# Optimization experiments

Hardware: AMD Instinct MI355X
Metric: run time of the kernel (lower is better)

Reference implementation:

```python
import jax, jax.numpy as jnp
import numpy as np

B, S, DIM, H, D = 2, 2048, 1024, 16, 64
WINDOW = 512
MAX_MEM_SEGMENTS = 1
ROPE_THETA = 10000.0


def _rope(t, pos):
    # lucidrains rotary-embedding-torch default: interleaved pairs
    d = t.shape[-1]
    inv_freq = 1.0 / (ROPE_THETA ** (jnp.arange(0, d, 2, dtype=jnp.float32) / d))
    freqs = pos[:, None].astype(jnp.float32) * inv_freq[None, :]        # [S, d/2]
    freqs = jnp.repeat(freqs, 2, axis=-1)                               # [S, d]
    cos, sin = jnp.cos(freqs), jnp.sin(freqs)
    t1, t2 = t[..., 0::2], t[..., 1::2]
    rot = jnp.stack((-t2, t1), axis=-1).reshape(t.shape)                # rotate_half
    return t * cos + rot * sin


def setup_inputs() -> dict:
    key = jax.random.key(0)
    ks = jax.random.split(key, 8)
    tokens = jax.random.normal(ks[0], (B, S, DIM), dtype=jnp.float32)
    value_residual = jax.random.normal(ks[1], (B, H, S, D), dtype=jnp.float32)
    episode_ids = jnp.sort(jax.random.randint(ks[2], (B, S), 0, 4), axis=-1)
    w = 0.02
    Wq = jax.random.normal(ks[3], (DIM, H * D), dtype=jnp.float32) * w
    Wkv = jax.random.normal(ks[4], (DIM, 2 * H * D), dtype=jnp.float32) * w
    Wo = jax.random.normal(ks[5], (H * D, DIM), dtype=jnp.float32) * w
    Wg = jax.random.normal(ks[6], (DIM, H), dtype=jnp.float32) * w
    Wmix = jax.random.normal(ks[7], (DIM, H), dtype=jnp.float32) * w
    return {"tokens": tokens, "value_residual": value_residual, "episode_ids": episode_ids,
            "Wq": Wq, "Wkv": Wkv, "Wo": Wo, "Wg": Wg, "Wmix": Wmix}


def reference(tokens, value_residual, episode_ids, Wq, Wkv, Wo, Wg, Wmix):
    b, s, _ = tokens.shape
    scale = D ** -0.5

    def split_heads(x):  # [b, n, h*d] -> [b, h, n, d]
        return x.reshape(b, s, H, D).transpose(0, 2, 1, 3)

    q = split_heads(tokens @ Wq)
    kv = tokens @ Wkv
    k, v = split_heads(kv[..., :H * D]), split_heads(kv[..., H * D:])

    q = q * scale

    # value-residual lerp: v.lerp(value_residual, mix)
    mix = jax.nn.sigmoid(jnp.einsum('bnd,dh->bhn', tokens, Wmix))[..., None]  # [b,h,n,1]
    v = v + mix * (value_residual - v)

    pos = jnp.arange(s)
    q = _rope(q, pos)
    k = _rope(k, pos)

    sim = jnp.einsum('bhid,bhjd->bhij', q, k)

    # fixed-window causal mask: masked where dist < 0 or dist > max_mem_segments*window
    dist = pos[:, None] - pos[None, :]
    win_mask = (dist < 0) | (dist > MAX_MEM_SEGMENTS * WINDOW)            # [s, s]
    ep_mask = episode_ids[:, :, None] != episode_ids[:, None, :]          # [b, s, s]
    mask = win_mask[None, None, :, :] | ep_mask[:, None, :, :]

    sim = jnp.where(mask, -jnp.finfo(sim.dtype).max, sim)
    attn = jax.nn.softmax(sim, axis=-1)
    out = jnp.einsum('bhij,bhjd->bhid', attn, v)

    # sigmoid value gating
    gate = jax.nn.sigmoid(jnp.einsum('bnd,dh->bhn', tokens, Wg))[..., None]
    out = out * gate

    out = out.transpose(0, 2, 1, 3).reshape(b, s, H * D)
    return out @ Wo
```

## Files before the change

### kernel.cpp

```cpp
#include <hip/hip_runtime.h>
#include <math.h>

#define BB 2
#define SS 2048
#define DIMM 1024
#define HH 16
#define DD 64
#define WINDOW 512

typedef __bf16 bf16x8 __attribute__((ext_vector_type(8)));
typedef float f32x4 __attribute__((ext_vector_type(4)));

__device__ __forceinline__ unsigned short f2bf(float f) {
    unsigned int u = __float_as_uint(f);
    u = (u + 0x7FFFu + ((u >> 16) & 1u)) >> 16;
    return (unsigned short)u;
}
__device__ __forceinline__ float bf2f(unsigned short u) {
    return __uint_as_float((unsigned int)u << 16);
}

__device__ __forceinline__ void async_cp16(unsigned short* lds_dst, const unsigned short* g_src) {
    __builtin_amdgcn_global_load_lds(
        (const __attribute__((address_space(1))) unsigned int*)g_src,
        (__attribute__((address_space(3))) unsigned int*)lds_dst, 16, 0, 0);
}

__global__ __launch_bounds__(256) void cvt_bf16_kernel(
    const float* __restrict__ src, unsigned short* __restrict__ dst, int n4)
{
    for (int i = blockIdx.x * 256 + threadIdx.x; i < n4; i += gridDim.x * 256) {
        float4 v = ((const float4*)src)[i];
        ushort4 o;
        o.x = f2bf(v.x); o.y = f2bf(v.y); o.z = f2bf(v.z); o.w = f2bf(v.w);
        ((ushort4*)dst)[i] = o;
    }
}

__global__ __launch_bounds__(256) void transpose_cvt3_kernel(
    const float* __restrict__ Wq, const float* __restrict__ Wkv,
    const float* __restrict__ Wo, unsigned short* __restrict__ BtW,
    unsigned short* __restrict__ WotW)
{
    int z = blockIdx.z;
    const float* src = (z == 0) ? Wq : (z == 1) ? Wkv : Wo;
    unsigned short* dst = (z == 0) ? BtW : (z == 1) ? (BtW + 1024 * 1024) : WotW;
    int C = (z == 1) ? 2048 : 1024;
    if (blockIdx.x * 32 >= C) return;
    const int R = 1024;

    __shared__ float t[32][33];
    int c0 = blockIdx.x * 32, r0 = blockIdx.y * 32;
    int tx = threadIdx.x & 31, ty = threadIdx.x >> 5;
    #pragma unroll
    for (int u = 0; u < 4; ++u)
        t[ty + 8 * u][tx] = src[(size_t)(r0 + ty + 8 * u) * C + c0 + tx];
    __syncthreads();
    #pragma unroll
    for (int u = 0; u < 4; ++u)
        dst[(size_t)(c0 + ty + 8 * u) * R + r0 + tx] = f2bf(t[tx][ty + 8 * u]);
}

__global__ __launch_bounds__(256) void build_wgmt_kernel(
    const float* __restrict__ Wg, const float* __restrict__ Wmix,
    unsigned short* __restrict__ dst)
{
    int idx = blockIdx.x * 256 + threadIdx.x;
    int n = idx >> 10, k = idx & 1023;
    const float* src = (n < 16) ? Wg : Wmix;
    dst[idx] = f2bf(src[k * HH + (n & 15)]);
}

__global__ __launch_bounds__(256) void mixgate_mfma(
    const unsigned short* __restrict__ A,
    const unsigned short* __restrict__ Bt,
    float* __restrict__ gate, float* __restrict__ mix)
{
    int mbase = blockIdx.x * 16;
    int tid = threadIdx.x;
    int wave = tid >> 6, lane = tid & 63;
    int fr = lane & 15, hi = lane >> 4;
    int kw = wave * 256;

    __shared__ float red[4][16][32];

    f32x4 acc[2];
    acc[0] = (f32x4){0.f, 0.f, 0.f, 0.f};
    acc[1] = (f32x4){0.f, 0.f, 0.f, 0.f};

    const unsigned short* a0 = A + (size_t)(mbase + fr) * 1024 + kw + hi * 8;
    const unsigned short* b0 = Bt + (size_t)fr * 1024 + kw + hi * 8;
    const unsigned short* b1 = Bt + (size_t)(16 + fr) * 1024 + kw + hi * 8;

    #pragma unroll 2
    for (int k = 0; k < 256; k += 32) {
        bf16x8 af0 = *(const bf16x8*)(a0 + k);
        bf16x8 bf0 = *(const bf16x8*)(b0 + k);
        bf16x8 bf1 = *(const bf16x8*)(b1 + k);
        acc[0] = __builtin_amdgcn_mfma_f32_16x16x32_bf16(af0, bf0, acc[0], 0, 0, 0);
        acc[1] = __builtin_amdgcn_mfma_f32_16x16x32_bf16(af0, bf1, acc[1], 0, 0, 0);
    }

    #pragma unroll
    for (int n_ = 0; n_ < 2; ++n_)
        #pragma unroll
        for (int j = 0; j < 4; ++j)
            red[wave][hi * 4 + j][n_ * 16 + fr] = acc[n_][j];
    __syncthreads();

    #pragma unroll
    for (int e = 0; e < 2; ++e) {
        int idx = tid * 2 + e;
        int r = idx >> 5, c = idx & 31;
        float s4 = red[0][r][c] + red[1][r][c] + red[2][r][c] + red[3][r][c];
        float sg = 1.f / (1.f + __expf(-s4));
        int mg = mbase + r;
        int b = mg >> 11, s = mg & 2047;
        int h = c & 15;
        float* dst = (c < 16) ? gate : mix;
        dst[((size_t)b * HH + h) * SS + s] = sg;
    }
}

__global__ __launch_bounds__(256) void epstart_kernel(
    const int* __restrict__ ep, int* __restrict__ epstart)
{
    int idx = blockIdx.x * 256 + threadIdx.x;
    int b = idx >> 11, i = idx & 2047;
    const int* e = ep + b * SS;
    int v = e[i];
    int lo = 0, hi = i;
    while (lo < hi) {
        int mid = (lo + hi) >> 1;
        if (e[mid] == v) hi = mid; else lo = mid + 1;
    }
    epstart[idx] = lo;
}

template<int EPI, int BM, int BN>
__global__ __launch_bounds__(256) void gemm_mfma(
    const unsigned short* __restrict__ A, const unsigned short* __restrict__ Bt,
    void* __restrict__ o0v, void* __restrict__ o1v, void* __restrict__ o2v)
{
    const int K = 1024;
    const int NT = 32;
    constexpr int MFR = BM / 32;
    constexpr int NFR = BN / 32;
    constexpr int LPS = (BM == 128 ? 2 : 1) + (BN == 128 ? 2 : 1);

    int lin = blockIdx.y * gridDim.x + blockIdx.x;
    int cpx = (gridDim.x * gridDim.y) >> 3;
    int swz = (lin & 7) * cpx + (lin >> 3);
    int nbase = (swz % gridDim.x) * BN;
    int mbase = (swz / gridDim.x) * BM;

    int tid = threadIdx.x;
    int lane = tid & 63;
    int wave = tid >> 6;
    int wr = wave >> 1, wc = wave & 1;
    int fr = lane & 15, hi = lane >> 4;

    __shared__ unsigned short As[3][BM * 32];
    __shared__ unsigned short Bs[3][BN * 32];

    int srow = tid >> 2;
    int sp   = tid & 3;
    int scol = (sp ^ ((srow >> 1) & 3)) * 8;
    const unsigned short* agp0 = A  + (size_t)(mbase + srow) * K + scol;
    const unsigned short* agp1 = (BM == 128)
        ? A + (size_t)(mbase + srow + 64) * K + scol : agp0;
    const unsigned short* bgp0 = Bt + (size_t)(nbase + srow) * K + scol;
    const unsigned short* bgp1 = (BN == 128)
        ? Bt + (size_t)(nbase + srow + 64) * K + scol : bgp0;

    f32x4 acc[MFR][NFR];
    #pragma unroll
    for (int m_ = 0; m_ < MFR; ++m_)
        #pragma unroll
        for (int n_ = 0; n_ < NFR; ++n_)
            acc[m_][n_] = (f32x4){0.f, 0.f, 0.f, 0.f};

    int aidx[MFR], bidx[NFR];
    #pragma unroll
    for (int m_ = 0; m_ < MFR; ++m_) {
        int row = wr * (BM / 2) + m_ * 16 + fr;
        aidx[m_] = row * 32 + (hi ^ ((row >> 1) & 3)) * 8;
    }
    #pragma unroll
    for (int n_ = 0; n_ < NFR; ++n_) {
        int row = wc * (BN / 2) + n_ * 16 + fr;
        bidx[n_] = row * 32 + (hi ^ ((row >> 1) & 3)) * 8;
    }

    auto stage = [&](int buf, int k0) {
        async_cp16(&As[buf][tid * 8], agp0 + k0);
        if constexpr (BM == 128)
            async_cp16(&As[buf][2048 + tid * 8], agp1 + k0);
        async_cp16(&Bs[buf][tid * 8], bgp0 + k0);
        if constexpr (BN == 128)
            async_cp16(&Bs[buf][2048 + tid * 8], bgp1 + k0);
    };
    auto compute = [&](int buf) {
        bf16x8 af[MFR], bfr[NFR];
        #pragma unroll
        for (int m_ = 0; m_ < MFR; ++m_) af[m_] = *(const bf16x8*)&As[buf][aidx[m_]];
        #pragma unroll
        for (int n_ = 0; n_ < NFR; ++n_) bfr[n_] = *(const bf16x8*)&Bs[buf][bidx[n_]];
        #pragma unroll
        for (int m_ = 0; m_ < MFR; ++m_)
            #pragma unroll
            for (int n_ = 0; n_ < NFR; ++n_)
                acc[m_][n_] = __builtin_amdgcn_mfma_f32_16x16x32_bf16(
                    af[m_], bfr[n_], acc[m_][n_], 0, 0, 0);
    };

    stage(0, 0); stage(1, 32);
    for (int t = 0; t < NT; ++t) {
        if (t + 1 < NT) {
            if constexpr (LPS == 4) asm volatile("s_waitcnt vmcnt(4)" ::: "memory");
            else if constexpr (LPS == 3) asm volatile("s_waitcnt vmcnt(3)" ::: "memory");
            else asm volatile("s_waitcnt vmcnt(2)" ::: "memory");
        } else {
            asm volatile("s_waitcnt vmcnt(0)" ::: "memory");
        }
        __builtin_amdgcn_s_barrier();
        if (t + 2 < NT) stage((t + 2) % 3, (t + 2) * 32);
        compute(t % 3);
    }

    #pragma unroll
    for (int m_ = 0; m_ < MFR; ++m_) {
        #pragma unroll
        for (int n_ = 0; n_ < NFR; ++n_) {
            int c = nbase + wc * (BN / 2) + n_ * 16 + fr;
            #pragma unroll
            for (int j = 0; j < 4; ++j) {
                int mg = mbase + wr * (BM / 2) + m_ * 16 + hi * 4 + j;
                float v = acc[m_][n_][j];
                if (EPI == 0) {
                    ((float*)o0v)[(size_t)mg * 1024 + c] = v;
                } else {
                    int b = mg >> 11, s = mg & 2047;
                    int cc = c & 1023, h = cc >> 6, d = cc & 63;
                    unsigned short* dst = (c < 1024) ? (unsigned short*)o0v
                                        : (c < 2048) ? (unsigned short*)o1v
                                                     : (unsigned short*)o2v;
                    dst[(((size_t)b * HH + h) * SS + s) * DD + d] = f2bf(v);
                }
            }
        }
    }
}

__global__ __launch_bounds__(256) void rope_lerp_kernel(
    unsigned short* __restrict__ q, unsigned short* __restrict__ k,
    const unsigned short* __restrict__ v0, const float* __restrict__ vres,
    const float* __restrict__ mix, unsigned short* __restrict__ vt)
{
    int st = blockIdx.x;
    int bh = blockIdx.y;
    int tid = threadIdx.x;
    int sl = tid >> 2;
    int dg = (tid & 3) * 16;
    int s = st * 64 + sl;
    size_t rowoff = ((size_t)bh * SS + s) * DD + dg;

    __shared__ unsigned short vtile[64][66];

    union { uint4 v[2]; unsigned short u[16]; } qa, ka, va;
    qa.v[0] = *(const uint4*)(q + rowoff);
    qa.v[1] = *(const uint4*)(q + rowoff + 8);
    ka.v[0] = *(const uint4*)(k + rowoff);
    ka.v[1] = *(const uint4*)(k + rowoff + 8);
    va.v[0] = *(const uint4*)(v0 + rowoff);
    va.v[1] = *(const uint4*)(v0 + rowoff + 8);
    float4 w[4];
    #pragma unroll
    for (int u = 0; u < 4; ++u) w[u] = *(const float4*)(vres + rowoff + 4 * u);
    float mx = mix[(size_t)bh * SS + s];

    #pragma unroll
    for (int u = 0; u < 8; ++u) {
        int d0 = dg + 2 * u;
        float inv_freq = powf(10000.f, -(float)d0 * (1.f / 64.f));
        float fr = (float)s * inv_freq;
        float red = fr - 6.2831853f * floorf(fr * 0.15915494f);
        float cs, sn;
        __sincosf(red, &sn, &cs);
        float x = bf2f(qa.u[2 * u]), y = bf2f(qa.u[2 * u + 1]);
        qa.u[2 * u]     = f2bf((x * cs - y * sn) * 0.125f);
        qa.u[2 * u + 1] = f2bf((y * cs + x * sn) * 0.125f);
        x = bf2f(ka.u[2 * u]); y = bf2f(ka.u[2 * u + 1]);
        ka.u[2 * u]     = f2bf(x * cs - y * sn);
        ka.u[2 * u + 1] = f2bf(y * cs + x * sn);
    }
    *(uint4*)(q + rowoff)     = qa.v[0];
    *(uint4*)(q + rowoff + 8) = qa.v[1];
    *(uint4*)(k + rowoff)     = ka.v[0];
    *(uint4*)(k + rowoff + 8) = ka.v[1];

    #pragma unroll
    for (int e = 0; e < 16; ++e) {
        float vv = bf2f(va.u[e]);
        float wr = ((const float*)w)[e];
        vtile[sl][dg + e] = f2bf(vv + mx * (wr - vv));
    }
    __syncthreads();

    int d = tid >> 2;
    int sseg = (tid & 3) * 16;
    union { uint4 v[2]; unsigned short u[16]; } ot;
    #pragma unroll
    for (int e = 0; e < 16; ++e) ot.u[e] = vtile[sseg + e][d];
    unsigned short* dst = vt + ((size_t)bh * DD + d) * SS + st * 64 + sseg;
    *(uint4*)dst = ot.v[0];
    *(uint4*)(dst + 8) = ot.v[1];
}

__global__ __launch_bounds__(256) void attn_mfma(
    const unsigned short* __restrict__ qbh, const unsigned short* __restrict__ kbh,
    const unsigned short* __restrict__ vt, const int* __restrict__ epstart,
    const float* __restrict__ gate, unsigned short* __restrict__ ao)
{
    int orig = blockIdx.x;
    int swz  = (orig & 7) * 128 + (orig >> 3);
    int bh = swz >> 5, qt = swz & 31;
    int b = bh >> 4, h = bh & 15;
    int q0 = qt * 64;
    int tid = threadIdx.x;
    int wave = tid >> 6, lane = tid & 63;
    int lq = lane & 15, lg = lane >> 4;
    int i = q0 + wave * 16 + lq;

    __shared__ unsigned short Ks[3][4096];
    __shared__ unsigned short Vs[3][4096];
    alignas(16) __shared__ unsigned short P_lds[4][16][72];

    int srow0 = tid >> 3, sch = tid & 7;
    int srow1 = srow0 + 32;
    int sc0 = ((sch ^ (srow0 & 7)) << 3);
    int sc1 = ((sch ^ (srow1 & 7)) << 3);
    const unsigned short* kS0 = kbh + ((size_t)bh * SS + srow0) * DD + sc0;
    const unsigned short* kS1 = kbh + ((size_t)bh * SS + srow1) * DD + sc1;
    const unsigned short* vS0 = vt + ((size_t)bh * DD + srow0) * SS + sc0;
    const unsigned short* vS1 = vt + ((size_t)bh * DD + srow1) * SS + sc1;

    auto stageKV = [&](int buf, int jbase) {
        async_cp16(&Ks[buf][tid * 8],        kS0 + (size_t)jbase * DD);
        async_cp16(&Ks[buf][2048 + tid * 8], kS1 + (size_t)jbase * DD);
        async_cp16(&Vs[buf][tid * 8],        vS0 + jbase);
        async_cp16(&Vs[buf][2048 + tid * 8], vS1 + jbase);
    };

    int fidx[4];
    #pragma unroll
    for (int n = 0; n < 4; ++n) {
        int r = 16 * n + lq;
        fidx[n] = r * 64 + ((lg ^ (r & 7)) << 3);
    }

    const unsigned short* qrow = qbh + ((size_t)bh * SS + i) * DD + lg * 8;
    bf16x8 bq0 = *(const bf16x8*)qrow;
    bf16x8 bq1 = *(const bf16x8*)(qrow + 32);

    int jmin = i - WINDOW;
    int es = epstart[b * SS + i];
    if (es > jmin) jmin = es;
    float gi = gate[(size_t)bh * SS + i];

    float m = -1e30f, l = 0.f;
    f32x4 o[4];
    #pragma unroll
    for (int n = 0; n < 4; ++n) o[n] = (f32x4){0.f, 0.f, 0.f, 0.f};

    int t0 = (qt < 8) ? (8 - qt) : 0;
    int nt = 9 - t0;
    int jb0 = 64 * (qt - 8 + t0);

    stageKV(0, jb0);
    if (nt > 1) stageKV(1, jb0 + 64);

    for (int u = 0; u < nt; ++u) {
        if (u + 1 < nt) asm volatile("s_waitcnt vmcnt(4)" ::: "memory");
        else            asm volatile("s_waitcnt vmcnt(0)" ::: "memory");
        __builtin_amdgcn_s_barrier();
        if (u + 2 < nt) stageKV((u + 2) % 3, jb0 + 64 * (u + 2));
        int buf = u % 3;
        int jbase = jb0 + 64 * u;

        f32x4 acc[4];
        #pragma unroll
        for (int n = 0; n < 4; ++n) acc[n] = (f32x4){0.f, 0.f, 0.f, 0.f};
        #pragma unroll
        for (int n = 0; n < 4; ++n) {
            bf16x8 kf0 = *(const bf16x8*)&Ks[buf][fidx[n]];
            bf16x8 kf1 = *(const bf16x8*)&Ks[buf][fidx[n] ^ 32];
            acc[n] = __builtin_amdgcn_mfma_f32_16x16x32_bf16(kf0, bq0, acc[n], 0, 0, 0);
            acc[n] = __builtin_amdgcn_mfma_f32_16x16x32_bf16(kf1, bq1, acc[n], 0, 0, 0);
        }

        int jb = jbase + lg * 4;
        #pragma unroll
        for (int n = 0; n < 4; ++n)
            #pragma unroll
            for (int r = 0; r < 4; ++r) {
                int j = jb + 16 * n + r;
                if (j < jmin || j > i) acc[n][r] = -3e38f;
            }

        float tm = -3e38f;
        #pragma unroll
        for (int n = 0; n < 4; ++n)
            tm = fmaxf(tm, fmaxf(fmaxf(acc[n][0], acc[n][1]), fmaxf(acc[n][2], acc[n][3])));
        tm = fmaxf(tm, __shfl_xor(tm, 16, 64));
        tm = fmaxf(tm, __shfl_xor(tm, 32, 64));
        float mnew = fmaxf(m, tm);
        float scale = __expf(m - mnew);
        float ts = 0.f;
        #pragma unroll
        for (int n = 0; n < 4; ++n)
            #pragma unroll
            for (int r = 0; r < 4; ++r) {
                float p = __expf(acc[n][r] - mnew);
                acc[n][r] = p;
                ts += p;
            }
        ts += __shfl_xor(ts, 16, 64);
        ts += __shfl_xor(ts, 32, 64);
        l = l * scale + ts;
        m = mnew;
        #pragma unroll
        for (int n = 0; n < 4; ++n) o[n] = o[n] * scale;

        #pragma unroll
        for (int n = 0; n < 4; ++n) {
            ushort4 u4;
            u4.x = f2bf(acc[n][0]); u4.y = f2bf(acc[n][1]);
            u4.z = f2bf(acc[n][2]); u4.w = f2bf(acc[n][3]);
            *(ushort4*)&P_lds[wave][lq][16 * n + lg * 4] = u4;
        }
        bf16x8 bp0 = *(const bf16x8*)&P_lds[wave][lq][lg * 8];
        bf16x8 bp1 = *(const bf16x8*)&P_lds[wave][lq][32 + lg * 8];

        #pragma unroll
        for (int n = 0; n < 4; ++n) {
            bf16x8 vf0 = *(const bf16x8*)&Vs[buf][fidx[n]];
            bf16x8 vf1 = *(const bf16x8*)&Vs[buf][fidx[n] ^ 32];
            o[n] = __builtin_amdgcn_mfma_f32_16x16x32_bf16(vf0, bp0, o[n], 0, 0, 0);
            o[n] = __builtin_amdgcn_mfma_f32_16x16x32_bf16(vf1, bp1, o[n], 0, 0, 0);
        }
    }

    float g = gi / l;
    #pragma unroll
    for (int n = 0; n < 4; ++n) {
        ushort4 u4;
        u4.x = f2bf(o[n][0] * g); u4.y = f2bf(o[n][1] * g);
        u4.z = f2bf(o[n][2] * g); u4.w = f2bf(o[n][3] * g);
        *(ushort4*)(ao + (((size_t)b * SS + i) * HH + h) * DD + 16 * n + lg * 4) = u4;
    }
}

extern "C" void kernel_launch(void* const* d_in, const int* in_sizes, int n_in,
                              void* d_out, int out_size, void* d_ws, size_t ws_size,
                              hipStream_t stream)
{
    const float* tokens = (const float*)d_in[0];
    const float* vres   = (const float*)d_in[1];
    const int*   ep     = (const int*)d_in[2];
    const float* Wq     = (const float*)d_in[3];
    const float* Wkv    = (const float*)d_in[4];
    const float* Wo     = (const float*)d_in[5];
    const float* Wg     = (const float*)d_in[6];
    const float* Wmix   = (const float*)d_in[7];
    float* out = (float*)d_out;

    char* wsb = (char*)d_ws;
    unsigned short* qbh  = (unsigned short*)(wsb + 0);
    unsigned short* kbh  = (unsigned short*)(wsb + 8388608);
    unsigned short* vb0  = (unsigned short*)(wsb + 16777216);
    unsigned short* vtb  = (unsigned short*)(wsb + 25165824);
    unsigned short* aob  = (unsigned short*)(wsb + 33554432);
    unsigned short* tokA = (unsigned short*)(wsb + 41943040);
    unsigned short* BtW  = (unsigned short*)(wsb + 50331648);
    float* gatep = (float*)(wsb + 56623104);
    float* mixp  = (float*)(wsb + 56885248);
    int*   epst  = (int*)(wsb + 57147392);
    unsigned short* wgmt = (unsigned short*)(wsb + 57163776);
    unsigned short* WotW = (unsigned short*)(wsb + 57229312);

    cvt_bf16_kernel<<<2048, 256, 0, stream>>>(tokens, tokA, (BB * SS * DIMM) / 4);
    transpose_cvt3_kernel<<<dim3(64, 32, 3), 256, 0, stream>>>(Wq, Wkv, Wo, BtW, WotW);
    build_wgmt_kernel<<<128, 256, 0, stream>>>(Wg, Wmix, wgmt);
    epstart_kernel<<<16, 256, 0, stream>>>(ep, epst);

    mixgate_mfma<<<256, 256, 0, stream>>>(tokA, wgmt, gatep, mixp);
    gemm_mfma<1, 128, 128><<<dim3(24, 32), 256, 0, stream>>>(tokA, BtW, qbh, kbh, vb0);
    rope_lerp_kernel<<<dim3(SS / 64, BB * HH), 256, 0, stream>>>(qbh, kbh, vb0, vres, mixp, vtb);
    attn_mfma<<<1024, 256, 0, stream>>>(qbh, kbh, vtb, epst, gatep, aob);

    gemm_mfma<0, 64, 64><<<dim3(16, 64), 256, 0, stream>>>(aob, WotW, out, nullptr, nullptr);
}
```

Baseline: 133.9 us.

## Merge small prep kernels and simplify GEMM pipeline to double buffering

Three small preprocessing kernels (token bf16 conversion, gate/mix weight packing, episode-start search) become one launch with block-range dispatch, saving two launches. The GEMM drops its triple-buffered LDS pipeline with explicit vmcnt waits and the block-index swizzle, and uses plain double buffering with __syncthreads. The output projection tile changes from 64x64 to 128x64. Less load/compute overlap and no L2-friendly swizzle could slow the GEMMs, while launch overhead goes down.

```diff
diff --git a/kernel.cpp b/kernel.cpp
--- a/kernel.cpp
+++ b/kernel.cpp
@@ -26,14 +26,38 @@
         (__attribute__((address_space(3))) unsigned int*)lds_dst, 16, 0, 0);
 }
 
-__global__ __launch_bounds__(256) void cvt_bf16_kernel(
-    const float* __restrict__ src, unsigned short* __restrict__ dst, int n4)
-{
-    for (int i = blockIdx.x * 256 + threadIdx.x; i < n4; i += gridDim.x * 256) {
-        float4 v = ((const float4*)src)[i];
-        ushort4 o;
-        o.x = f2bf(v.x); o.y = f2bf(v.y); o.z = f2bf(v.z); o.w = f2bf(v.w);
-        ((ushort4*)dst)[i] = o;
+__global__ __launch_bounds__(256) void prep_kernel(
+    const float* __restrict__ tokens, unsigned short* __restrict__ tokA,
+    const float* __restrict__ Wg, const float* __restrict__ Wmix,
+    unsigned short* __restrict__ wgmt,
+    const int* __restrict__ ep, int* __restrict__ epstart)
+{
+    int bid = blockIdx.x;
+    int tid = threadIdx.x;
+    if (bid < 2048) {
+        const int n4 = (BB * SS * DIMM) / 4;
+        for (int i = bid * 256 + tid; i < n4; i += 2048 * 256) {
+            float4 v = ((const float4*)tokens)[i];
+            ushort4 o;
+            o.x = f2bf(v.x); o.y = f2bf(v.y); o.z = f2bf(v.z); o.w = f2bf(v.w);
+            ((ushort4*)tokA)[i] = o;
+        }
+    } else if (bid < 2176) {
+        int idx = (bid - 2048) * 256 + tid;
+        int n = idx >> 10, k = idx & 1023;
+        const float* src = (n < 16) ? Wg : Wmix;
+        wgmt[idx] = f2bf(src[k * HH + (n & 15)]);
+    } else {
+        int idx = (bid - 2176) * 256 + tid;
+        int b = idx >> 11, i = idx & 2047;
+        const int* e = ep + b * SS;
+        int v = e[i];
+        int lo = 0, hi = i;
+        while (lo < hi) {
+            int mid = (lo + hi) >> 1;
+            if (e[mid] == v) hi = mid; else lo = mid + 1;
+        }
+        epstart[idx] = lo;
     }
 }
 
@@ -59,16 +83,6 @@
     #pragma unroll
     for (int u = 0; u < 4; ++u)
         dst[(size_t)(c0 + ty + 8 * u) * R + r0 + tx] = f2bf(t[tx][ty + 8 * u]);
-}
-
-__global__ __launch_bounds__(256) void build_wgmt_kernel(
-    const float* __restrict__ Wg, const float* __restrict__ Wmix,
-    unsigned short* __restrict__ dst)
-{
-    int idx = blockIdx.x * 256 + threadIdx.x;
-    int n = idx >> 10, k = idx & 1023;
-    const float* src = (n < 16) ? Wg : Wmix;
-    dst[idx] = f2bf(src[k * HH + (n & 15)]);
 }
 
 __global__ __launch_bounds__(256) void mixgate_mfma(
@@ -122,37 +136,16 @@
     }
 }
 
-__global__ __launch_bounds__(256) void epstart_kernel(
-    const int* __restrict__ ep, int* __restrict__ epstart)
-{
-    int idx = blockIdx.x * 256 + threadIdx.x;
-    int b = idx >> 11, i = idx & 2047;
-    const int* e = ep + b * SS;
-    int v = e[i];
-    int lo = 0, hi = i;
-    while (lo < hi) {
-        int mid = (lo + hi) >> 1;
-        if (e[mid] == v) hi = mid; else lo = mid + 1;
-    }
-    epstart[idx] = lo;
-}
-
 template<int EPI, int BM, int BN>
 __global__ __launch_bounds__(256) void gemm_mfma(
     const unsigned short* __restrict__ A, const unsigned short* __restrict__ Bt,
     void* __restrict__ o0v, void* __restrict__ o1v, void* __restrict__ o2v)
 {
     const int K = 1024;
-    const int NT = 32;
     constexpr int MFR = BM / 32;
     constexpr int NFR = BN / 32;
-    constexpr int LPS = (BM == 128 ? 2 : 1) + (BN == 128 ? 2 : 1);
-
-    int lin = blockIdx.y * gridDim.x + blockIdx.x;
-    int cpx = (gridDim.x * gridDim.y) >> 3;
-    int swz = (lin & 7) * cpx + (lin >> 3);
-    int nbase = (swz % gridDim.x) * BN;
-    int mbase = (swz / gridDim.x) * BM;
+    int nbase = blockIdx.x * BN;
+    int mbase = blockIdx.y * BM;
 
     int tid = threadIdx.x;
     int lane = tid & 63;
@@ -160,8 +153,8 @@
     int wr = wave >> 1, wc = wave & 1;
     int fr = lane & 15, hi = lane >> 4;
 
-    __shared__ unsigned short As[3][BM * 32];
-    __shared__ unsigned short Bs[3][BN * 32];
+    __shared__ unsigned short As[2][BM * 32];
+    __shared__ unsigned short Bs[2][BN * 32];
 
     int srow = tid >> 2;
     int sp   = tid & 3;
@@ -200,32 +193,24 @@
         if constexpr (BN == 128)
             async_cp16(&Bs[buf][2048 + tid * 8], bgp1 + k0);
     };
-    auto compute = [&](int buf) {
+
+    stage(0, 0);
+    for (int k0 = 0; k0 < K; k0 += 32) {
+        int cur = (k0 >> 5) & 1;
+        __syncthreads();
+        if (k0 + 32 < K) stage(cur ^ 1, k0 + 32);
+
         bf16x8 af[MFR], bfr[NFR];
         #pragma unroll
-        for (int m_ = 0; m_ < MFR; ++m_) af[m_] = *(const bf16x8*)&As[buf][aidx[m_]];
-        #pragma unroll
-        for (int n_ = 0; n_ < NFR; ++n_) bfr[n_] = *(const bf16x8*)&Bs[buf][bidx[n_]];
+        for (int m_ = 0; m_ < MFR; ++m_) af[m_] = *(const bf16x8*)&As[cur][aidx[m_]];
+        #pragma unroll
+        for (int n_ = 0; n_ < NFR; ++n_) bfr[n_] = *(const bf16x8*)&Bs[cur][bidx[n_]];
         #pragma unroll
         for (int m_ = 0; m_ < MFR; ++m_)
             #pragma unroll
             for (int n_ = 0; n_ < NFR; ++n_)
                 acc[m_][n_] = __builtin_amdgcn_mfma_f32_16x16x32_bf16(
                     af[m_], bfr[n_], acc[m_][n_], 0, 0, 0);
-    };
-
-    stage(0, 0); stage(1, 32);
-    for (int t = 0; t < NT; ++t) {
-        if (t + 1 < NT) {
-            if constexpr (LPS == 4) asm volatile("s_waitcnt vmcnt(4)" ::: "memory");
-            else if constexpr (LPS == 3) asm volatile("s_waitcnt vmcnt(3)" ::: "memory");
-            else asm volatile("s_waitcnt vmcnt(2)" ::: "memory");
-        } else {
-            asm volatile("s_waitcnt vmcnt(0)" ::: "memory");
-        }
-        __builtin_amdgcn_s_barrier();
-        if (t + 2 < NT) stage((t + 2) % 3, (t + 2) * 32);
-        compute(t % 3);
     }
 
     #pragma unroll
@@ -489,15 +474,13 @@
     unsigned short* wgmt = (unsigned short*)(wsb + 57163776);
     unsigned short* WotW = (unsigned short*)(wsb + 57229312);
 
-    cvt_bf16_kernel<<<2048, 256, 0, stream>>>(tokens, tokA, (BB * SS * DIMM) / 4);
+    prep_kernel<<<2192, 256, 0, stream>>>(tokens, tokA, Wg, Wmix, wgmt, ep, epst);
     transpose_cvt3_kernel<<<dim3(64, 32, 3), 256, 0, stream>>>(Wq, Wkv, Wo, BtW, WotW);
-    build_wgmt_kernel<<<128, 256, 0, stream>>>(Wg, Wmix, wgmt);
-    epstart_kernel<<<16, 256, 0, stream>>>(ep, epst);
 
     mixgate_mfma<<<256, 256, 0, stream>>>(tokA, wgmt, gatep, mixp);
     gemm_mfma<1, 128, 128><<<dim3(24, 32), 256, 0, stream>>>(tokA, BtW, qbh, kbh, vb0);
     rope_lerp_kernel<<<dim3(SS / 64, BB * HH), 256, 0, stream>>>(qbh, kbh, vb0, vres, mixp, vtb);
     attn_mfma<<<1024, 256, 0, stream>>>(qbh, kbh, vtb, epst, gatep, aob);
 
-    gemm_mfma<0, 64, 64><<<dim3(16, 64), 256, 0, stream>>>(aob, WotW, out, nullptr, nullptr);
-}
+    gemm_mfma<0, 128, 64><<<dim3(16, 32), 256, 0, stream>>>(aob, WotW, out, nullptr, nullptr);
+}
```

New measurement: 126.7 us. 5.4% less time.
